# Optimization experiments

Hardware: AMD Instinct MI355X
Metric: run time of the kernel (lower is better)

## Reference

```python
import jax, jax.numpy as jnp
import numpy as np

EMBED_DIM = 128
TEMP_DIM = EMBED_DIM // 4  # 32
NUM_TYPES = 50
DATE_SCALE = 1825.0
LN_EPS = 1e-5


def _layernorm(x, w, b):
    m = jnp.mean(x, axis=-1, keepdims=True)
    v = jnp.mean((x - m) ** 2, axis=-1, keepdims=True)
    return (x - m) * jax.lax.rsqrt(v + LN_EPS) * w + b


def setup_inputs() -> dict:
    key = jax.random.key(0)
    ks = jax.random.split(key, 16)
    B, L = 4096, 200
    inp = {
        "treatment_ids": jax.random.randint(ks[0], (B, L), 0, NUM_TYPES, dtype=jnp.int64 if jax.config.jax_enable_x64 else jnp.int32),
        "dates": jax.random.uniform(ks[1], (B, L), dtype=jnp.float32) * DATE_SCALE,
        "lengths": jax.random.randint(ks[2], (B,), 0, L + 1, dtype=jnp.int32),
        # parameters
        "emb": jax.random.normal(ks[3], (NUM_TYPES, EMBED_DIM), jnp.float32),
        "tp_w": jax.random.normal(ks[4], (1, TEMP_DIM), jnp.float32) * 0.1,
        "tp_b": jnp.zeros((TEMP_DIM,), jnp.float32),
        "tp_lnw": jnp.ones((TEMP_DIM,), jnp.float32),
        "tp_lnb": jnp.zeros((TEMP_DIM,), jnp.float32),
        "w1": jax.random.normal(ks[5], (EMBED_DIM + TEMP_DIM, EMBED_DIM), jnp.float32) * 0.05,
        "b1": jnp.zeros((EMBED_DIM,), jnp.float32),
        "ln1w": jnp.ones((EMBED_DIM,), jnp.float32),
        "ln1b": jnp.zeros((EMBED_DIM,), jnp.float32),
        "w2": jax.random.normal(ks[6], (EMBED_DIM, EMBED_DIM), jnp.float32) * 0.05,
        "b2": jnp.zeros((EMBED_DIM,), jnp.float32),
        "ln2w": jnp.ones((EMBED_DIM,), jnp.float32),
        "ln2b": jnp.zeros((EMBED_DIM,), jnp.float32),
    }
    return inp


def reference(treatment_ids, dates, lengths, emb, tp_w, tp_b, tp_lnw, tp_lnb,
              w1, b1, ln1w, ln1b, w2, b2, ln2w, ln2b):
    B, L = treatment_ids.shape
    mask = (jnp.arange(L)[None, :] < lengths[:, None]).astype(dates.dtype)  # [B, L]

    # embedding lookup [B, L, D]
    treat = emb[treatment_ids]

    # temporal projection: Linear(1 -> D/4) + LN + GELU
    dn = (dates / DATE_SCALE)[..., None]                      # [B, L, 1]
    temporal = dn * tp_w[0] + tp_b                            # [B, L, D/4]
    temporal = jax.nn.gelu(_layernorm(temporal, tp_lnw, tp_lnb), approximate=False)

    combined = jnp.concatenate([treat, temporal], axis=-1)    # [B, L, D + D/4]

    # sequence encoder (dropout is identity at eval)
    h = jnp.einsum("blk,kd->bld", combined, w1) + b1
    h = jax.nn.gelu(_layernorm(h, ln1w, ln1b), approximate=False)
    h = jnp.einsum("blk,kd->bld", h, w2) + b2
    h = _layernorm(h, ln2w, ln2b)                             # [B, L, D]

    # masked mean pool; empty histories -> zeros
    counts = jnp.sum(mask, axis=1, keepdims=True)             # [B, 1]
    pooled = jnp.sum(h * mask[..., None], axis=1) / jnp.maximum(counts, 1.0)
    return jnp.where(counts > 0, pooled, 0.0)                 # [B, D]
```

## Files before the change

### kernel.cpp

```cpp
#include <hip/hip_runtime.h>
#include <cmath>

#define LN_EPS 1e-5f

typedef float  f32x4  __attribute__((ext_vector_type(4)));
typedef short  short8 __attribute__((ext_vector_type(8)));
typedef unsigned int uint4v __attribute__((ext_vector_type(4)));

#define W1TF_U4 512
#define W2F_U4  2048
#define E1_U4   1650
#define WLDS_U4 2560

__device__ __forceinline__ unsigned short f32_bf16_rne(float f) {
    union { float f; unsigned u; } v; v.f = f;
    unsigned r = v.u + 0x7FFFu + ((v.u >> 16) & 1u);
    return (unsigned short)(r >> 16);
}

__device__ __forceinline__ unsigned cvt_pk_bf16(float lo, float hi) {
    unsigned r;
    asm("v_cvt_pk_bf16_f32 %0, %1, %2" : "=v"(r) : "v"(lo), "v"(hi));
    return r;
}

__device__ __forceinline__ float gelu_f(float x) {
    const float arg = x * fmaf(x * x, 0.044715f, 1.0f);
    const float e   = __builtin_amdgcn_exp2f(arg * -2.302258f);
    const float r   = __builtin_amdgcn_rcpf(e + 1.0f);
    return x * r;
}

template<int C>
__device__ __forceinline__ float dpp_radd(float x) {
    int t = __builtin_amdgcn_update_dpp(0, __builtin_bit_cast(int, x), C, 0xF, 0xF, true);
    return x + __builtin_bit_cast(float, t);
}
__device__ __forceinline__ float red16(float x) {
    x = dpp_radd<0x128>(x);
    x = dpp_radd<0x124>(x);
    x = dpp_radd<0x122>(x);
    x = dpp_radd<0x121>(x);
    return x;
}

__global__ void prep_kernel(const float* __restrict__ w1, const float* __restrict__ w2,
                            const float* __restrict__ emb, const float* __restrict__ b1,
                            const float* __restrict__ tp_w, const float* __restrict__ tp_b,
                            unsigned* __restrict__ ws) {
    const int tid = blockIdx.x * 256 + threadIdx.x;
    uint4v* w1tf = (uint4v*)ws;
    uint4v* w2f  = w1tf + W1TF_U4;
    float*  E1   = (float*)(w2f + W2F_U4);
    float*  tps  = E1 + 6600;

    for (int i = tid; i < W1TF_U4; i += 8192) {
        const int lane = i & 63, nt = i >> 6;
        const int k0 = 128 + (lane >> 4) * 8, n = nt * 16 + (lane & 15);
        uint4v r;
        #pragma unroll
        for (int j2 = 0; j2 < 4; ++j2) {
            unsigned lo = f32_bf16_rne(w1[(k0 + 2 * j2) * 128 + n]);
            unsigned hi = f32_bf16_rne(w1[(k0 + 2 * j2 + 1) * 128 + n]);
            r[j2] = lo | (hi << 16);
        }
        w1tf[i] = r;
    }
    for (int i = tid; i < W2F_U4; i += 8192) {
        const int lane = i & 63, nt = (i >> 6) & 7, kt = i >> 9;
        const int k0 = kt * 32 + (lane >> 4) * 8, n = nt * 16 + (lane & 15);
        uint4v r;
        #pragma unroll
        for (int j2 = 0; j2 < 4; ++j2) {
            unsigned lo = f32_bf16_rne(w2[(k0 + 2 * j2) * 128 + n]);
            unsigned hi = f32_bf16_rne(w2[(k0 + 2 * j2 + 1) * 128 + n]);
            r[j2] = lo | (hi << 16);
        }
        w2f[i] = r;
    }
    if (tid < 6400) {
        const int t = tid >> 7, n = tid & 127;
        float s = b1[n];
        #pragma unroll 4
        for (int k = 0; k < 128; ++k)
            s = fmaf(emb[t * 128 + k], w1[k * 128 + n], s);
        E1[t * 132 + n] = s;
    }
    if (tid == 0) {
        float Sw = 0.f, Sb = 0.f, Sww = 0.f, Swb = 0.f, Sbb = 0.f;
        for (int j = 0; j < 32; ++j) {
            const float ww = tp_w[j], bb = tp_b[j];
            Sw += ww; Sb += bb; Sww += ww * ww; Swb += ww * bb; Sbb += bb * bb;
        }
        tps[0] = Sw; tps[1] = Sb; tps[2] = Sww; tps[3] = Swb; tps[4] = Sbb;
    }
}

__global__ __launch_bounds__(768, 3) void encoder_mfma(
    const int*   __restrict__ tids,  const float* __restrict__ dates,
    const int*   __restrict__ lengths,
    const float* __restrict__ tp_w,  const float* __restrict__ tp_b,
    const float* __restrict__ tp_lnw,const float* __restrict__ tp_lnb,
    const float* __restrict__ b1,    const float* __restrict__ ln1w, const float* __restrict__ ln1b,
    const float* __restrict__ b2,    const float* __restrict__ ln2w, const float* __restrict__ ln2b,
    const unsigned* __restrict__ ws, float* __restrict__ out,
    int B, int L)
{
    __shared__ __align__(16) uint4v wlds[WLDS_U4];
    __shared__ __align__(16) float  E1lds[6600];
    __shared__ __align__(16) unsigned short a2[12][4][64][8];
    __shared__ float poolbuf[3][12][128];
    __shared__ __align__(16) f32x4 tcoef[32];
    __shared__ __align__(16) f32x4 ecoef1[128];
    __shared__ __align__(16) f32x4 ecoef2[128];

    const int tid = threadIdx.x;
    const int lane = tid & 63, w = tid >> 6;
    const int c = lane & 15, g = lane >> 4;
    const int b0 = blockIdx.x * 3;

    for (int i = tid; i < WLDS_U4; i += 768)
        wlds[i] = ((const uint4v*)ws)[i];
    for (int i = tid; i < E1_U4; i += 768)
        ((uint4v*)E1lds)[i] = ((const uint4v*)ws)[WLDS_U4 + i];

    const float* tps = (const float*)((const uint4v*)ws + WLDS_U4 + E1_U4);

    if (tid < 32)  tcoef[tid]  = (f32x4){tp_w[tid], tp_b[tid], tp_lnw[tid], tp_lnb[tid]};
    if (tid < 128) {
        ecoef1[tid] = (f32x4){0.f, ln1w[tid], ln1b[tid], 0.f};
        ecoef2[tid] = (f32x4){b2[tid], ln2w[tid], ln2b[tid], 0.f};
    }
    __syncthreads();

    const float Sw = tps[0], Sb = tps[1], Sww = tps[2], Swb = tps[3], Sbb = tps[4];

    const int len0 = (b0 + 0 < B) ? min(max(lengths[b0 + 0], 0), L) : 0;
    const int len1 = (b0 + 1 < B) ? min(max(lengths[b0 + 1], 0), L) : 0;
    const int len2 = (b0 + 2 < B) ? min(max(lengths[b0 + 2], 0), L) : 0;
    const int nt0 = (len0 + 15) >> 4, nt1 = (len1 + 15) >> 4, nt2 = (len2 + 15) >> 4;
    const int cum1 = nt0, cum2 = nt0 + nt1, T = cum2 + nt2;

    float pool0[8], pool1[8], pool2[8];
    #pragma unroll
    for (int nt = 0; nt < 8; ++nt) { pool0[nt] = 0.f; pool1[nt] = 0.f; pool2[nt] = 0.f; }
    const int srl = lane ^ ((lane >> 3) & 3);

    for (int t = w; t < T; t += 12) {
        const int row  = (t >= cum2) ? 2 : ((t >= cum1) ? 1 : 0);
        const int tl   = t - ((row == 2) ? cum2 : ((row == 1) ? cum1 : 0));
        const int bb   = b0 + row;
        const int lenr = (row == 2) ? len2 : ((row == 1) ? len1 : len0);
        const int R0   = tl << 4;
        const long base = (long)bb * L;

        const int pc = min(R0 + c, L - 1);
        const float d = dates[base + pc] * (1.f / 1825.f);
        int idr[4];
        #pragma unroll
        for (int r = 0; r < 4; ++r)
            idr[r] = tids[base + min(R0 + 4 * g + r, L - 1)];

        short8 tfrag;
        {
            const float tm = fmaf(d, Sw, Sb) * (1.f / 32.f);
            float tv = fmaf(d * d, Sww, fmaf(2.f * d, Swb, Sbb)) * (1.f / 32.f) - tm * tm;
            const float trs = rsqrtf(fmaxf(tv, 0.f) + LN_EPS);
            const int j0 = g * 8;
            uint4v r;
            #pragma unroll
            for (int j2 = 0; j2 < 4; ++j2) {
                const f32x4 t0 = tcoef[j0 + 2*j2];
                const f32x4 t1 = tcoef[j0 + 2*j2 + 1];
                const float y0 = fmaf((fmaf(d, t0[0], t0[1]) - tm) * trs, t0[2], t0[3]);
                const float y1 = fmaf((fmaf(d, t1[0], t1[1]) - tm) * trs, t1[2], t1[3]);
                r[j2] = cvt_pk_bf16(gelu_f(y0), gelu_f(y1));
            }
            union { uint4v u; short8 s; } cv; cv.u = r;
            tfrag = cv.s;
        }

        f32x4 acc[8];
        #pragma unroll
        for (int r = 0; r < 4; ++r) {
            const int e1base = idr[r] * 132 + c;
            #pragma unroll
            for (int nt = 0; nt < 8; ++nt)
                acc[nt][r] = E1lds[e1base + nt * 16];
        }
        __builtin_amdgcn_s_setprio(1);
        #pragma unroll
        for (int nt = 0; nt < 8; ++nt) {
            const short8 bf = ((const short8*)wlds)[nt * 64 + lane];
            acc[nt] = __builtin_amdgcn_mfma_f32_16x16x32_bf16(tfrag, bf, acc[nt], 0, 0, 0);
        }
        __builtin_amdgcn_s_setprio(0);

        {
            f32x4 e1[8];
            #pragma unroll
            for (int nt = 0; nt < 8; ++nt) e1[nt] = ecoef1[nt * 16 + c];
            #pragma unroll
            for (int r = 0; r < 4; ++r) {
                float v[8], s = 0.f, q = 0.f;
                #pragma unroll
                for (int nt = 0; nt < 8; ++nt) {
                    v[nt] = acc[nt][r];
                    s += v[nt]; q = fmaf(v[nt], v[nt], q);
                }
                s = red16(s); q = red16(q);
                const float mean = s * (1.f / 128.f);
                const float var  = fmaxf(q * (1.f / 128.f) - mean * mean, 0.f);
                const float rstd = rsqrtf(var + LN_EPS);
                const int mrow = 4 * g + r;
                #pragma unroll
                for (int n2 = 0; n2 < 4; ++n2) {
                    const float y0 = gelu_f(fmaf((v[2*n2]   - mean) * rstd, e1[2*n2][1],   e1[2*n2][2]));
                    const float y1 = gelu_f(fmaf((v[2*n2+1] - mean) * rstd, e1[2*n2+1][1], e1[2*n2+1][2]));
                    const unsigned pk = cvt_pk_bf16(y0, y1);
                    {
                        const int kcol  = (2*n2) * 16 + c;
                        const int row64 = ((kcol >> 3) & 3) * 16 + mrow;
                        const int srow  = row64 ^ ((row64 >> 3) & 3);
                        a2[w][kcol >> 5][srow][kcol & 7] = (unsigned short)(pk & 0xffffu);
                    }
                    {
                        const int kcol  = (2*n2+1) * 16 + c;
                        const int row64 = ((kcol >> 3) & 3) * 16 + mrow;
                        const int srow  = row64 ^ ((row64 >> 3) & 3);
                        a2[w][kcol >> 5][srow][kcol & 7] = (unsigned short)(pk >> 16);
                    }
                }
            }
        }

        asm volatile("" ::: "memory");

        f32x4 acc2[8];
        #pragma unroll
        for (int nt = 0; nt < 8; ++nt) acc2[nt] = (f32x4){0.f, 0.f, 0.f, 0.f};
        __builtin_amdgcn_s_setprio(1);
        #pragma unroll
        for (int kt2 = 0; kt2 < 4; ++kt2) {
            short8 af;
            __builtin_memcpy(&af, &a2[w][kt2][srl][0], 16);
            #pragma unroll
            for (int nt = 0; nt < 8; ++nt) {
                const short8 bf = ((const short8*)(wlds + W1TF_U4))[(kt2 * 8 + nt) * 64 + lane];
                acc2[nt] = __builtin_amdgcn_mfma_f32_16x16x32_bf16(af, bf, acc2[nt], 0, 0, 0);
            }
        }
        __builtin_amdgcn_s_setprio(0);

        asm volatile("" ::: "memory");

        {
            f32x4 e2[8];
            #pragma unroll
            for (int nt = 0; nt < 8; ++nt) e2[nt] = ecoef2[nt * 16 + c];
            float ptile[8];
            #pragma unroll
            for (int nt = 0; nt < 8; ++nt) ptile[nt] = 0.f;
            #pragma unroll
            for (int r = 0; r < 4; ++r) {
                float v[8], s = 0.f, q = 0.f;
                #pragma unroll
                for (int nt = 0; nt < 8; ++nt) {
                    v[nt] = acc2[nt][r] + e2[nt][0];
                    s += v[nt]; q = fmaf(v[nt], v[nt], q);
                }
                s = red16(s); q = red16(q);
                const float mean = s * (1.f / 128.f);
                const float var  = fmaxf(q * (1.f / 128.f) - mean * mean, 0.f);
                const float rstd = rsqrtf(var + LN_EPS);
                const float msk = ((R0 + 4 * g + r) < lenr) ? 1.f : 0.f;
                #pragma unroll
                for (int nt = 0; nt < 8; ++nt) {
                    const float y = fmaf((v[nt] - mean) * rstd, e2[nt][1], e2[nt][2]);
                    ptile[nt] = fmaf(y, msk, ptile[nt]);
                }
            }
            if (row == 0) {
                #pragma unroll
                for (int nt = 0; nt < 8; ++nt) pool0[nt] += ptile[nt];
            } else if (row == 1) {
                #pragma unroll
                for (int nt = 0; nt < 8; ++nt) pool1[nt] += ptile[nt];
            } else {
                #pragma unroll
                for (int nt = 0; nt < 8; ++nt) pool2[nt] += ptile[nt];
            }
        }
    }

    #pragma unroll
    for (int nt = 0; nt < 8; ++nt) {
        float t0 = pool0[nt]; t0 += __shfl_xor(t0, 16); t0 += __shfl_xor(t0, 32); pool0[nt] = t0;
        float t1 = pool1[nt]; t1 += __shfl_xor(t1, 16); t1 += __shfl_xor(t1, 32); pool1[nt] = t1;
        float t2 = pool2[nt]; t2 += __shfl_xor(t2, 16); t2 += __shfl_xor(t2, 32); pool2[nt] = t2;
    }
    if (g == 0) {
        #pragma unroll
        for (int nt = 0; nt < 8; ++nt) {
            poolbuf[0][w][nt * 16 + c] = pool0[nt];
            poolbuf[1][w][nt * 16 + c] = pool1[nt];
            poolbuf[2][w][nt * 16 + c] = pool2[nt];
        }
    }
    __syncthreads();
    if (tid < 384) {
        const int r3  = tid >> 7;
        const int col = tid & 127;
        const int bo  = b0 + r3;
        if (bo < B) {
            const int lenb = min(max(lengths[bo], 0), L);
            float s = 0.f;
            #pragma unroll
            for (int k = 0; k < 12; ++k) s += poolbuf[r3][k][col];
            out[bo * 128 + col] = (lenb > 0) ? s / (float)lenb : 0.f;
        }
    }
}

extern "C" void kernel_launch(void* const* d_in, const int* in_sizes, int n_in,
                              void* d_out, int out_size, void* d_ws, size_t ws_size,
                              hipStream_t stream) {
    const int*   tids    = (const int*)  d_in[0];
    const float* dates   = (const float*)d_in[1];
    const int*   lengths = (const int*)  d_in[2];
    const float* emb     = (const float*)d_in[3];
    const float* tp_w    = (const float*)d_in[4];
    const float* tp_b    = (const float*)d_in[5];
    const float* tp_lnw  = (const float*)d_in[6];
    const float* tp_lnb  = (const float*)d_in[7];
    const float* w1      = (const float*)d_in[8];
    const float* b1      = (const float*)d_in[9];
    const float* ln1w    = (const float*)d_in[10];
    const float* ln1b    = (const float*)d_in[11];
    const float* w2      = (const float*)d_in[12];
    const float* b2      = (const float*)d_in[13];
    const float* ln2w    = (const float*)d_in[14];
    const float* ln2b    = (const float*)d_in[15];
    float* out = (float*)d_out;

    const int B = in_sizes[2];
    const int L = in_sizes[0] / B;

    hipLaunchKernelGGL(prep_kernel, dim3(32), dim3(256), 0, stream,
                       w1, w2, emb, b1, tp_w, tp_b, (unsigned*)d_ws);
    hipLaunchKernelGGL(encoder_mfma, dim3((B + 2) / 3), dim3(768), 0, stream,
                       tids, dates, lengths, tp_w, tp_b, tp_lnw, tp_lnb,
                       b1, ln1w, ln1b, b2, ln2w, ln2b,
                       (const unsigned*)d_ws, out, B, L);
}
```

Baseline: 195.2 us.

## Prefetch next tile ids/dates, vectorize E1 gathers, fold LN2 affine into pooling

Next-tile treatment ids and dates are now loaded one iteration ahead, so the global-load latency overlaps the current tile's MFMA work. The E1 table is re-laid out with a per-column stride of 12, so each lane gathers its 8 values with two 16-byte LDS reads instead of eight scalar reads. The b2 bias now initialises the second GEMM accumulator. The LN2 scale and shift are applied after summing the masked rows, which removes per-element affine work. This costs more LDS for E1 and a few extra registers.

```diff
diff --git a/kernel.cpp b/kernel.cpp
--- a/kernel.cpp
+++ b/kernel.cpp
@@ -4,12 +4,13 @@
 #define LN_EPS 1e-5f
 
 typedef float  f32x4  __attribute__((ext_vector_type(4)));
+typedef float  f32x2  __attribute__((ext_vector_type(2)));
 typedef short  short8 __attribute__((ext_vector_type(8)));
 typedef unsigned int uint4v __attribute__((ext_vector_type(4)));
 
 #define W1TF_U4 512
 #define W2F_U4  2048
-#define E1_U4   1650
+#define E1_U4   2450
 #define WLDS_U4 2560
 
 __device__ __forceinline__ unsigned short f32_bf16_rne(float f) {
@@ -52,7 +53,7 @@
     uint4v* w1tf = (uint4v*)ws;
     uint4v* w2f  = w1tf + W1TF_U4;
     float*  E1   = (float*)(w2f + W2F_U4);
-    float*  tps  = E1 + 6600;
+    float*  tps  = E1 + 9800;
 
     for (int i = tid; i < W1TF_U4; i += 8192) {
         const int lane = i & 63, nt = i >> 6;
@@ -84,7 +85,7 @@
         #pragma unroll 4
         for (int k = 0; k < 128; ++k)
             s = fmaf(emb[t * 128 + k], w1[k * 128 + n], s);
-        E1[t * 132 + n] = s;
+        E1[t * 196 + (n & 15) * 12 + (n >> 4)] = s;
     }
     if (tid == 0) {
         float Sw = 0.f, Sb = 0.f, Sww = 0.f, Swb = 0.f, Sbb = 0.f;
@@ -107,12 +108,12 @@
     int B, int L)
 {
     __shared__ __align__(16) uint4v wlds[WLDS_U4];
-    __shared__ __align__(16) float  E1lds[6600];
+    __shared__ __align__(16) float  E1lds[9800];
     __shared__ __align__(16) unsigned short a2[12][4][64][8];
     __shared__ float poolbuf[3][12][128];
     __shared__ __align__(16) f32x4 tcoef[32];
     __shared__ __align__(16) f32x4 ecoef1[128];
-    __shared__ __align__(16) f32x4 ecoef2[128];
+    __shared__ __align__(8)  f32x2 ecoef2[128];
 
     const int tid = threadIdx.x;
     const int lane = tid & 63, w = tid >> 6;
@@ -129,8 +130,11 @@
     if (tid < 32)  tcoef[tid]  = (f32x4){tp_w[tid], tp_b[tid], tp_lnw[tid], tp_lnb[tid]};
     if (tid < 128) {
         ecoef1[tid] = (f32x4){0.f, ln1w[tid], ln1b[tid], 0.f};
-        ecoef2[tid] = (f32x4){b2[tid], ln2w[tid], ln2b[tid], 0.f};
-    }
+        ecoef2[tid] = (f32x2){ln2w[tid], ln2b[tid]};
+    }
+    float b2c[8];
+    #pragma unroll
+    for (int nt = 0; nt < 8; ++nt) b2c[nt] = b2[nt * 16 + c];
     __syncthreads();
 
     const float Sw = tps[0], Sb = tps[1], Sww = tps[2], Swb = tps[3], Sbb = tps[4];
@@ -146,20 +150,38 @@
     for (int nt = 0; nt < 8; ++nt) { pool0[nt] = 0.f; pool1[nt] = 0.f; pool2[nt] = 0.f; }
     const int srl = lane ^ ((lane >> 3) & 3);
 
+    int pidr[4]; float pd = 0.f;
+    if (w < T) {
+        const int row0 = (w >= cum2) ? 2 : ((w >= cum1) ? 1 : 0);
+        const int tl0  = w - ((row0 == 2) ? cum2 : ((row0 == 1) ? cum1 : 0));
+        const long bs0 = (long)(b0 + row0) * L;
+        const int R00  = tl0 << 4;
+        pd = dates[bs0 + min(R00 + c, L - 1)] * (1.f / 1825.f);
+        #pragma unroll
+        for (int r = 0; r < 4; ++r)
+            pidr[r] = tids[bs0 + min(R00 + 4 * g + r, L - 1)];
+    }
+
     for (int t = w; t < T; t += 12) {
         const int row  = (t >= cum2) ? 2 : ((t >= cum1) ? 1 : 0);
         const int tl   = t - ((row == 2) ? cum2 : ((row == 1) ? cum1 : 0));
-        const int bb   = b0 + row;
         const int lenr = (row == 2) ? len2 : ((row == 1) ? len1 : len0);
         const int R0   = tl << 4;
-        const long base = (long)bb * L;
-
-        const int pc = min(R0 + c, L - 1);
-        const float d = dates[base + pc] * (1.f / 1825.f);
+
         int idr[4];
         #pragma unroll
-        for (int r = 0; r < 4; ++r)
-            idr[r] = tids[base + min(R0 + 4 * g + r, L - 1)];
+        for (int r = 0; r < 4; ++r) idr[r] = pidr[r];
+        const float d = pd;
+
+        f32x4 acc[8];
+        #pragma unroll
+        for (int r = 0; r < 4; ++r) {
+            const float* p = &E1lds[idr[r] * 196 + c * 12];
+            const f32x4 lo = *(const f32x4*)p;
+            const f32x4 hi = *(const f32x4*)(p + 4);
+            acc[0][r] = lo[0]; acc[1][r] = lo[1]; acc[2][r] = lo[2]; acc[3][r] = lo[3];
+            acc[4][r] = hi[0]; acc[5][r] = hi[1]; acc[6][r] = hi[2]; acc[7][r] = hi[3];
+        }
 
         short8 tfrag;
         {
@@ -180,14 +202,6 @@
             tfrag = cv.s;
         }
 
-        f32x4 acc[8];
-        #pragma unroll
-        for (int r = 0; r < 4; ++r) {
-            const int e1base = idr[r] * 132 + c;
-            #pragma unroll
-            for (int nt = 0; nt < 8; ++nt)
-                acc[nt][r] = E1lds[e1base + nt * 16];
-        }
         __builtin_amdgcn_s_setprio(1);
         #pragma unroll
         for (int nt = 0; nt < 8; ++nt) {
@@ -195,6 +209,20 @@
             acc[nt] = __builtin_amdgcn_mfma_f32_16x16x32_bf16(tfrag, bf, acc[nt], 0, 0, 0);
         }
         __builtin_amdgcn_s_setprio(0);
+
+        {
+            const int tn = t + 12;
+            if (tn < T) {
+                const int rowN = (tn >= cum2) ? 2 : ((tn >= cum1) ? 1 : 0);
+                const int tlN  = tn - ((rowN == 2) ? cum2 : ((rowN == 1) ? cum1 : 0));
+                const long bsN = (long)(b0 + rowN) * L;
+                const int R0N  = tlN << 4;
+                pd = dates[bsN + min(R0N + c, L - 1)] * (1.f / 1825.f);
+                #pragma unroll
+                for (int r = 0; r < 4; ++r)
+                    pidr[r] = tids[bsN + min(R0N + 4 * g + r, L - 1)];
+            }
+        }
 
         {
             f32x4 e1[8];
@@ -238,7 +266,8 @@
 
         f32x4 acc2[8];
         #pragma unroll
-        for (int nt = 0; nt < 8; ++nt) acc2[nt] = (f32x4){0.f, 0.f, 0.f, 0.f};
+        for (int nt = 0; nt < 8; ++nt)
+            acc2[nt] = (f32x4){b2c[nt], b2c[nt], b2c[nt], b2c[nt]};
         __builtin_amdgcn_s_setprio(1);
         #pragma unroll
         for (int kt2 = 0; kt2 < 4; ++kt2) {
@@ -255,40 +284,47 @@
         asm volatile("" ::: "memory");
 
         {
-            f32x4 e2[8];
-            #pragma unroll
-            for (int nt = 0; nt < 8; ++nt) e2[nt] = ecoef2[nt * 16 + c];
-            float ptile[8];
-            #pragma unroll
-            for (int nt = 0; nt < 8; ++nt) ptile[nt] = 0.f;
+            float A[8], Sbv = 0.f, Sgv = 0.f;
+            #pragma unroll
+            for (int nt = 0; nt < 8; ++nt) A[nt] = 0.f;
             #pragma unroll
             for (int r = 0; r < 4; ++r) {
-                float v[8], s = 0.f, q = 0.f;
-                #pragma unroll
-                for (int nt = 0; nt < 8; ++nt) {
-                    v[nt] = acc2[nt][r] + e2[nt][0];
-                    s += v[nt]; q = fmaf(v[nt], v[nt], q);
+                float s = 0.f, q = 0.f;
+                #pragma unroll
+                for (int nt = 0; nt < 8; ++nt) {
+                    const float v = acc2[nt][r];
+                    s += v; q = fmaf(v, v, q);
                 }
                 s = red16(s); q = red16(q);
                 const float mean = s * (1.f / 128.f);
                 const float var  = fmaxf(q * (1.f / 128.f) - mean * mean, 0.f);
                 const float rstd = rsqrtf(var + LN_EPS);
-                const float msk = ((R0 + 4 * g + r) < lenr) ? 1.f : 0.f;
-                #pragma unroll
-                for (int nt = 0; nt < 8; ++nt) {
-                    const float y = fmaf((v[nt] - mean) * rstd, e2[nt][1], e2[nt][2]);
-                    ptile[nt] = fmaf(y, msk, ptile[nt]);
-                }
+                const float msk  = ((R0 + 4 * g + r) < lenr) ? 1.f : 0.f;
+                const float alf  = msk * rstd;
+                Sbv = fmaf(alf, mean, Sbv);
+                Sgv += msk;
+                #pragma unroll
+                for (int nt = 0; nt < 8; ++nt)
+                    A[nt] = fmaf(acc2[nt][r], alf, A[nt]);
             }
             if (row == 0) {
                 #pragma unroll
-                for (int nt = 0; nt < 8; ++nt) pool0[nt] += ptile[nt];
+                for (int nt = 0; nt < 8; ++nt) {
+                    const f32x2 e = ecoef2[nt * 16 + c];
+                    pool0[nt] = fmaf(e[0], A[nt] - Sbv, fmaf(e[1], Sgv, pool0[nt]));
+                }
             } else if (row == 1) {
                 #pragma unroll
-                for (int nt = 0; nt < 8; ++nt) pool1[nt] += ptile[nt];
+                for (int nt = 0; nt < 8; ++nt) {
+                    const f32x2 e = ecoef2[nt * 16 + c];
+                    pool1[nt] = fmaf(e[0], A[nt] - Sbv, fmaf(e[1], Sgv, pool1[nt]));
+                }
             } else {
                 #pragma unroll
-                for (int nt = 0; nt < 8; ++nt) pool2[nt] += ptile[nt];
+                for (int nt = 0; nt < 8; ++nt) {
+                    const f32x2 e = ecoef2[nt * 16 + c];
+                    pool2[nt] = fmaf(e[0], A[nt] - Sbv, fmaf(e[1], Sgv, pool2[nt]));
+                }
             }
         }
     }
```

New measurement: 191.1 us. 2.1% less time.
